# Performance work log

Hardware: AMD Instinct MI355X
Metric: run time of the kernel (lower is better)

## Reference

```python
import jax, jax.numpy as jnp
import numpy as np

B, T, D, M, H = 2048, 64, 4, 4, 256
N_STEPS = 32

# Dopri5 Butcher tableau (5th-order solution weights; f is autonomous so c is unused)
A21 = 1.0 / 5.0
A31, A32 = 3.0 / 40.0, 9.0 / 40.0
A41, A42, A43 = 44.0 / 45.0, -56.0 / 15.0, 32.0 / 9.0
A51, A52, A53, A54 = 19372.0 / 6561.0, -25360.0 / 2187.0, 64448.0 / 6561.0, -212.0 / 729.0
A61, A62, A63, A64, A65 = 9017.0 / 3168.0, -355.0 / 33.0, 46732.0 / 5247.0, 49.0 / 176.0, -5103.0 / 18656.0
B1, B3, B4, B5, B6 = 35.0 / 384.0, 500.0 / 1113.0, 125.0 / 192.0, -2187.0 / 6784.0, 11.0 / 84.0


def _gru(xin, W_ih, W_hh, b_ih, b_hh):
    # PyTorch GRU cell, gate order (r, z, n), h0 = 0
    h0 = jnp.zeros((xin.shape[0], W_hh.shape[1]), xin.dtype)

    def step(h, xt):
        gx = xt @ W_ih.T + b_ih
        gh = h @ W_hh.T + b_hh
        xr, xz, xn = jnp.split(gx, 3, axis=-1)
        hr, hz, hn = jnp.split(gh, 3, axis=-1)
        r = jax.nn.sigmoid(xr + hr)
        z = jax.nn.sigmoid(xz + hz)
        n = jnp.tanh(xn + r * hn)
        return (1.0 - z) * n + z * h, None

    h, _ = jax.lax.scan(step, h0, jnp.swapaxes(xin, 0, 1))
    return h


def _ode_f(y, p):
    W1, b1, W2, b2, W3, b3, W4, b4 = p
    h = jax.nn.selu(y @ W1.T + b1)
    h = jax.nn.selu(h @ W2.T + b2)
    h = jax.nn.selu(h @ W3.T + b3)
    return h @ W4.T + b4


def _dopri5(y0, dt, p):
    # fixed-grid Dopri5; dt is per-sample (B,1)
    def step(y, _):
        k1 = _ode_f(y, p)
        k2 = _ode_f(y + dt * (A21 * k1), p)
        k3 = _ode_f(y + dt * (A31 * k1 + A32 * k2), p)
        k4 = _ode_f(y + dt * (A41 * k1 + A42 * k2 + A43 * k3), p)
        k5 = _ode_f(y + dt * (A51 * k1 + A52 * k2 + A53 * k3 + A54 * k4), p)
        k6 = _ode_f(y + dt * (A61 * k1 + A62 * k2 + A63 * k3 + A64 * k4 + A65 * k5), p)
        y_new = y + dt * (B1 * k1 + B3 * k3 + B4 * k4 + B5 * k5 + B6 * k6)
        return y_new, None

    y, _ = jax.lax.scan(step, y0, None, length=N_STEPS)
    return y


def setup_inputs() -> dict:
    key = jax.random.key(0)
    ks = jax.random.split(key, 16)
    inp = {
        'x': jax.random.normal(ks[0], (B, T, D), jnp.float32),
        'meta': jax.random.normal(ks[1], (B, M), jnp.float32),
        'W_ih': jax.random.normal(ks[2], (3 * H, D + M), jnp.float32) * 0.05,
        'W_hh': jax.random.normal(ks[3], (3 * H, H), jnp.float32) * 0.05,
        'b_ih': jnp.zeros((3 * H,), jnp.float32),
        'b_hh': jnp.zeros((3 * H,), jnp.float32),
        'enc_W1': jax.random.normal(ks[4], (H, H), jnp.float32) * 0.05,
        'enc_b1': jnp.zeros((H,), jnp.float32),
        'enc_W2': jax.random.normal(ks[5], (2 * H, H), jnp.float32) * 0.05,
        'enc_b2': jnp.zeros((2 * H,), jnp.float32),
        'ode_W1': jax.random.normal(ks[6], (H, H), jnp.float32) * 0.001,
        'ode_b1': jnp.full((H,), 0.5, jnp.float32),
        'ode_W2': jax.random.normal(ks[7], (H, H), jnp.float32) * 0.001,
        'ode_b2': jnp.full((H,), 0.5, jnp.float32),
        'ode_W3': jax.random.normal(ks[8], (H, H), jnp.float32) * 0.001,
        'ode_b3': jnp.full((H,), 0.5, jnp.float32),
        'ode_W4': jax.random.normal(ks[9], (H, H), jnp.float32) * 0.001,
        'ode_b4': jnp.full((H,), 0.5, jnp.float32),
        'out_W': jax.random.normal(ks[10], (1, H + M), jnp.float32) * 0.05,
        'out_b': jnp.zeros((1,), jnp.float32),
    }
    return inp


def reference(x, meta, W_ih, W_hh, b_ih, b_hh, enc_W1, enc_b1, enc_W2, enc_b2,
              ode_W1, ode_b1, ode_W2, ode_b2, ode_W3, ode_b3, ode_W4, ode_b4,
              out_W, out_b):
    Bsz, Ts = x.shape[0], x.shape[1]
    Hd = enc_W1.shape[0]
    meta_t = jnp.broadcast_to(meta[:, None, :], (Bsz, Ts, meta.shape[1]))
    xin = jnp.concatenate([x, meta_t], axis=-1)  # (B, T, D+M)
    h = _gru(xin, W_ih, W_hh, b_ih, b_hh)        # (B, H)
    h = jax.nn.relu(h @ enc_W1.T + enc_b1)
    out = h @ enc_W2.T + enc_b2                  # (B, 2H)
    mean, std = out[:, :Hd], out[:, Hd:]
    eps = jax.random.normal(jax.random.key(42), mean.shape, mean.dtype)
    y0 = eps * std + mean
    times = x[:, :, 0]
    dt = (times[:, -1:] - times[:, :1]) / N_STEPS  # (B, 1) per-sample step
    p = (ode_W1, ode_b1, ode_W2, ode_b2, ode_W3, ode_b3, ode_W4, ode_b4)
    yT = _dopri5(y0, dt, p)                      # (B, H) == sol.ys[:, -1, :]
    latent = jnp.concatenate([yT, meta], axis=-1)
    return latent @ out_W.T + out_b              # (B, 1)
```

## Files before the change

### kernel.cpp

```cpp
#include <hip/hip_runtime.h>
#include <math.h>

#define HD   256
#define RB   16
#define TB   1024
#define TT   64
#define NST  32
#define BSZ  2048

typedef __attribute__((ext_vector_type(8))) short short8;
typedef __attribute__((ext_vector_type(4))) float f32x4;
typedef unsigned short ushort_t;

__device__ __forceinline__ float sigmoidf_(float x) {
    return 1.0f / (1.0f + __expf(-x));
}
__device__ __forceinline__ float tanhf_(float x) {
    float e = __expf(2.0f * x);
    return 1.0f - 2.0f / (e + 1.0f);
}
__device__ __forceinline__ float seluf_(float x) {
    const float a = 1.6732632423543772f, s = 1.0507009873554805f;
    return x > 0.0f ? s * x : s * a * (__expf(x) - 1.0f);
}
__device__ __forceinline__ float erfinvf_(float x) {
    float w = -log1pf(-x * x);
    float p;
    if (w < 5.0f) {
        w -= 2.5f;
        p = 2.81022636e-08f;
        p = fmaf(p, w, 3.43273939e-07f);
        p = fmaf(p, w, -3.5233877e-06f);
        p = fmaf(p, w, -4.39150654e-06f);
        p = fmaf(p, w, 0.00021858087f);
        p = fmaf(p, w, -0.00125372503f);
        p = fmaf(p, w, -0.00417768164f);
        p = fmaf(p, w, 0.246640727f);
        p = fmaf(p, w, 1.50140941f);
    } else {
        w = sqrtf(w) - 3.0f;
        p = -0.000200214257f;
        p = fmaf(p, w, 0.000100950558f);
        p = fmaf(p, w, 0.00134934322f);
        p = fmaf(p, w, -0.00367342844f);
        p = fmaf(p, w, 0.00573950773f);
        p = fmaf(p, w, -0.0076224613f);
        p = fmaf(p, w, 0.00943887047f);
        p = fmaf(p, w, 1.00167406f);
        p = fmaf(p, w, 2.83297682f);
    }
    return p * x;
}

#define TF_ROUND(x0, x1, R) { x0 += x1; x1 = (x1 << (R)) | (x1 >> (32 - (R))); x1 ^= x0; }

__device__ __forceinline__ void threefry_(unsigned c0, unsigned c1, unsigned& r0, unsigned& r1) {
    const unsigned ks0 = 0u, ks1 = 42u, ks2 = 0x1BD11BDAu ^ 0u ^ 42u;
    unsigned x0 = c0 + ks0, x1 = c1 + ks1;
    TF_ROUND(x0,x1,13) TF_ROUND(x0,x1,15) TF_ROUND(x0,x1,26) TF_ROUND(x0,x1,6)
    x0 += ks1; x1 += ks2 + 1u;
    TF_ROUND(x0,x1,17) TF_ROUND(x0,x1,29) TF_ROUND(x0,x1,16) TF_ROUND(x0,x1,24)
    x0 += ks2; x1 += ks0 + 2u;
    TF_ROUND(x0,x1,13) TF_ROUND(x0,x1,15) TF_ROUND(x0,x1,26) TF_ROUND(x0,x1,6)
    x0 += ks0; x1 += ks1 + 3u;
    TF_ROUND(x0,x1,17) TF_ROUND(x0,x1,29) TF_ROUND(x0,x1,16) TF_ROUND(x0,x1,24)
    x0 += ks1; x1 += ks2 + 4u;
    TF_ROUND(x0,x1,13) TF_ROUND(x0,x1,15) TF_ROUND(x0,x1,26) TF_ROUND(x0,x1,6)
    x0 += ks2; x1 += ks0 + 5u;
    r0 = x0; r1 = x1;
}

__device__ __forceinline__ float jax_normal_(unsigned i) {
    unsigned o0, o1;
    threefry_(0u, i, o0, o1);
    unsigned bits = o0 ^ o1;
    unsigned fb = (bits >> 9) | 0x3F800000u;
    float f = __uint_as_float(fb) - 1.0f;
    const float lo = -0.99999994f;
    float u = f * 2.0f + lo;
    u = fmaxf(lo, u);
    return 1.41421356237f * erfinvf_(u);
}

__device__ __forceinline__ ushort_t f2bf(float f) {
    unsigned u = __float_as_uint(f);
    return (ushort_t)((u + 0x7FFFu + ((u >> 16) & 1u)) >> 16);
}
__device__ __forceinline__ float bf2f(ushort_t u) {
    return __uint_as_float(((unsigned)u) << 16);
}

__device__ __forceinline__ int midx(int row, int k) {
    int chunk = k >> 3;
    return row * 256 + (((chunk ^ (row & 7)) << 3) | (k & 7));
}

__device__ __forceinline__ short8 ldw_f32(const float* __restrict__ Wf, int row, int k0) {
    const float4 w0 = *(const float4*)(Wf + (size_t)row * 256 + k0);
    const float4 w1 = *(const float4*)(Wf + (size_t)row * 256 + k0 + 4);
    union { ushort_t u[8]; short8 v; } bb;
    bb.u[0] = f2bf(w0.x); bb.u[1] = f2bf(w0.y); bb.u[2] = f2bf(w0.z); bb.u[3] = f2bf(w0.w);
    bb.u[4] = f2bf(w1.x); bb.u[5] = f2bf(w1.y); bb.u[6] = f2bf(w1.z); bb.u[7] = f2bf(w1.w);
    return bb.v;
}

template<int WBF>
__device__ __forceinline__ f32x4 mfma_layer(const ushort_t* __restrict__ inbf,
                                            const ushort_t* __restrict__ Wp,
                                            const float* __restrict__ Wf,
                                            const int lm, const int kb,
                                            const int wv, const int l, const int jo)
{
    f32x4 acc = {0.f, 0.f, 0.f, 0.f};
    const ushort_t* wpl = Wp + (((size_t)wv * 8) * 64 + l) * 8;
#pragma unroll
    for (int kt = 0; kt < 8; ++kt) {
        const int k0 = kt * 32 + kb * 8;
        short8 a = *(const short8*)(inbf + midx(lm, k0));
        short8 b;
        if (WBF) b = *(const short8*)(wpl + kt * 512);
        else     b = ldw_f32(Wf, jo, k0);
        acc = __builtin_amdgcn_mfma_f32_16x16x32_bf16(a, b, acc, 0, 0, 0);
    }
    return acc;
}

__global__ void cvt_k(const float* __restrict__ o1, const float* __restrict__ o2,
                      const float* __restrict__ o3, const float* __restrict__ o4,
                      const float* __restrict__ whh, const float* __restrict__ e1,
                      const float* __restrict__ e2, ushort_t* __restrict__ out) {
    int i = blockIdx.x * blockDim.x + threadIdx.x;
    if (i >= 655360) return;
    int m = i >> 16, r = i & 65535;
    const float* src;
    switch (m) {
    case 0: src = o1; break;
    case 1: src = o2; break;
    case 2: src = o3; break;
    case 3: src = o4; break;
    case 4: src = whh; break;
    case 5: src = whh + 65536; break;
    case 6: src = whh + 131072; break;
    case 7: src = e1; break;
    case 8: src = e2; break;
    default: src = e2 + 65536; break;
    }
    int e  = r & 7;
    int l  = (r >> 3) & 63;
    int kt = (r >> 9) & 7;
    int nt = r >> 12;
    int srow = nt * 16 + (l & 15);
    int sk   = kt * 32 + (l >> 4) * 8 + e;
    out[i] = f2bf(src[srow * 256 + sk]);
}

template<int WBF>
__global__ __launch_bounds__(TB, 4) void fused_kernel(
    const float* __restrict__ x,
    const float* __restrict__ meta,
    const float* __restrict__ W_ih,
    const float* __restrict__ W_hh,
    const float* __restrict__ b_ih,
    const float* __restrict__ b_hh,
    const float* __restrict__ eW1,
    const float* __restrict__ eb1,
    const float* __restrict__ eW2,
    const float* __restrict__ eb2,
    const float* __restrict__ oW1, const float* __restrict__ ob1,
    const float* __restrict__ oW2, const float* __restrict__ ob2,
    const float* __restrict__ oW3, const float* __restrict__ ob3,
    const float* __restrict__ oW4, const float* __restrict__ ob4,
    const float* __restrict__ outW,
    const float* __restrict__ outb,
    const ushort_t* __restrict__ wsbf,
    float* __restrict__ out)
{
    const int tid = threadIdx.x;
    const int t8  = tid & 255;
    const int l   = tid & 63;
    const int wv  = tid >> 6;
    const int lm  = l & 15;
    const int kb  = l >> 4;
    const int jo  = wv * 16 + lm;
    const int er4 = l >> 4;
    const int b0  = blockIdx.x * RB;

    __shared__ float h0[RB][HD];
    __shared__ float xall[RB][TT * 4];
    __shared__ float red[TB];
    __shared__ __align__(16) ushort_t mir[4][RB][256];
    __shared__ ushort_t kstb[6][RB * 256];
    __shared__ float meta_s[RB][4];
    __shared__ float dt_s[RB];

    ushort_t* YBF = &mir[0][0][0];
    ushort_t* YTB = &mir[1][0][0];
    ushort_t* T1B = &mir[2][0][0];
    ushort_t* T2B = &mir[3][0][0];
    const ushort_t* wsO1  = wsbf;
    const ushort_t* wsO2  = wsbf + 65536;
    const ushort_t* wsO3  = wsbf + 131072;
    const ushort_t* wsO4  = wsbf + 196608;
    const ushort_t* wsWr  = wsbf + 262144;
    const ushort_t* wsWz  = wsbf + 327680;
    const ushort_t* wsWn  = wsbf + 393216;
    const ushort_t* wsE1  = wsbf + 458752;
    const ushort_t* wsE2m = wsbf + 524288;
    const ushort_t* wsE2s = wsbf + 589824;

#pragma unroll
    for (int i = 0; i < 4; ++i) {
        int idx = tid + i * TB;
        int r = idx >> 8, c = idx & 255;
        xall[r][c] = x[(size_t)(b0 + r) * 256 + c];
        h0[r][c] = 0.0f;
    }
    if (tid < RB * 4) { int r = tid >> 2, mm = tid & 3; meta_s[r][mm] = meta[(b0 + r) * 4 + mm]; }
    {
        unsigned* mz = (unsigned*)&mir[0][0][0];
#pragma unroll
        for (int i = 0; i < 8; ++i) mz[tid + i * TB] = 0u;
    }
    __syncthreads();
    if (tid < RB) dt_s[tid] = (xall[tid][TT * 4 - 4] - xall[tid][0]) * (1.0f / (float)NST);

    float wxr[4], wxz[4], wxn[4];
#pragma unroll
    for (int d = 0; d < 4; ++d) {
        wxr[d] = W_ih[(size_t)jo * 8 + d];
        wxz[d] = W_ih[(size_t)(jo + 256) * 8 + d];
        wxn[d] = W_ih[(size_t)(jo + 512) * 8 + d];
    }
    float base_r[4], base_z[4], base_xn[4];
    {
        float mwr[4], mwz[4], mwn[4];
#pragma unroll
        for (int mm = 0; mm < 4; ++mm) {
            mwr[mm] = W_ih[(size_t)jo * 8 + 4 + mm];
            mwz[mm] = W_ih[(size_t)(jo + 256) * 8 + 4 + mm];
            mwn[mm] = W_ih[(size_t)(jo + 512) * 8 + 4 + mm];
        }
        const float bir = b_ih[jo], biz = b_ih[jo + 256], bin_ = b_ih[jo + 512];
        const float bhr = b_hh[jo], bhz = b_hh[jo + 256];
#pragma unroll
        for (int r = 0; r < 4; ++r) {
            const int R = er4 * 4 + r;
            float sr = bir + bhr, sz = biz + bhz, sn = bin_;
#pragma unroll
            for (int mm = 0; mm < 4; ++mm) {
                float mv = meta_s[R][mm];
                sr = fmaf(mv, mwr[mm], sr);
                sz = fmaf(mv, mwz[mm], sz);
                sn = fmaf(mv, mwn[mm], sn);
            }
            base_r[r] = sr; base_z[r] = sz; base_xn[r] = sn;
        }
    }
    const float bhn = b_hh[512 + jo];

    const ushort_t* wrl = wsWr + (((size_t)wv * 8) * 64 + l) * 8;
    const ushort_t* wzl = wsWz + (((size_t)wv * 8) * 64 + l) * 8;
    const ushort_t* wnl = wsWn + (((size_t)wv * 8) * 64 + l) * 8;
    int p = 0;
#pragma unroll 1
    for (int t = 0; t < TT; ++t) {
        const ushort_t* YHp = &mir[p][0][0];
        f32x4 aR = {0.f,0.f,0.f,0.f}, aZ = {0.f,0.f,0.f,0.f}, aN = {0.f,0.f,0.f,0.f};
#pragma unroll 2
        for (int kt = 0; kt < 8; ++kt) {
            const int k0 = kt * 32 + kb * 8;
            short8 a = *(const short8*)(YHp + midx(lm, k0));
            short8 b;
            if (WBF) b = *(const short8*)(wrl + kt * 512);
            else     b = ldw_f32(W_hh, jo, k0);
            aR = __builtin_amdgcn_mfma_f32_16x16x32_bf16(a, b, aR, 0, 0, 0);
            if (WBF) b = *(const short8*)(wzl + kt * 512);
            else     b = ldw_f32(W_hh, jo + 256, k0);
            aZ = __builtin_amdgcn_mfma_f32_16x16x32_bf16(a, b, aZ, 0, 0, 0);
            if (WBF) b = *(const short8*)(wnl + kt * 512);
            else     b = ldw_f32(W_hh, jo + 512, k0);
            aN = __builtin_amdgcn_mfma_f32_16x16x32_bf16(a, b, aN, 0, 0, 0);
        }
        {
            ushort_t* YHn = &mir[p ^ 1][0][0];
#pragma unroll
            for (int r = 0; r < 4; ++r) {
                const int R = er4 * 4 + r;
                float xr = base_r[r], xz = base_z[r], xn = base_xn[r];
#pragma unroll
                for (int d = 0; d < 4; ++d) {
                    float xv = xall[R][t * 4 + d];
                    xr = fmaf(xv, wxr[d], xr);
                    xz = fmaf(xv, wxz[d], xz);
                    xn = fmaf(xv, wxn[d], xn);
                }
                float rg = sigmoidf_(xr + aR[r]);
                float zg = sigmoidf_(xz + aZ[r]);
                float ng = tanhf_(fmaf(rg, aN[r] + bhn, xn));
                float hp = h0[R][jo];
                float hnew = fmaf(zg, hp - ng, ng);
                h0[R][jo] = hnew;
                YHn[midx(R, jo)] = f2bf(hnew);
            }
        }
        __syncthreads();
        p ^= 1;
    }

    {
        f32x4 acc = mfma_layer<WBF>(YBF, wsE1, eW1, lm, kb, wv, l, jo);
        {
            const float eb1j = eb1[jo];
#pragma unroll
            for (int r = 0; r < 4; ++r)
                T1B[midx(er4 * 4 + r, jo)] = f2bf(fmaxf(acc[r] + eb1j, 0.0f));
        }
        __syncthreads();

        f32x4 aM = mfma_layer<WBF>(T1B, wsE2m, eW2, lm, kb, wv, l, jo);
        f32x4 aS = mfma_layer<WBF>(T1B, wsE2s, eW2 + 65536, lm, kb, wv, l, jo);
        {
            const float bm = eb2[jo], bs = eb2[256 + jo];
#pragma unroll
            for (int r = 0; r < 4; ++r) {
                const int row = er4 * 4 + r;
                float e = jax_normal_((unsigned)((b0 + row) * HD + jo));
                float y0v = fmaf(e, aS[r] + bs, aM[r] + bm);
                h0[row][jo] = y0v;
                YBF[midx(row, jo)] = f2bf(y0v);
            }
        }
        __syncthreads();
    }

    const float A21 = (float)(1.0/5.0);
    const float A31 = (float)(3.0/40.0),      A32 = (float)(9.0/40.0);
    const float A41 = (float)(44.0/45.0),     A42 = (float)(-56.0/15.0),    A43 = (float)(32.0/9.0);
    const float A51 = (float)(19372.0/6561.0),A52 = (float)(-25360.0/2187.0),
                A53 = (float)(64448.0/6561.0),A54 = (float)(-212.0/729.0);
    const float A61 = (float)(9017.0/3168.0), A62 = (float)(-355.0/33.0),
                A63 = (float)(46732.0/5247.0),A64 = (float)(49.0/176.0),    A65 = (float)(-5103.0/18656.0);
    const float B1f = (float)(35.0/384.0),    B3f = (float)(500.0/1113.0),  B4f = (float)(125.0/192.0),
                B5f = (float)(-2187.0/6784.0),B6f = (float)(11.0/84.0);

    const float o1b = ob1[jo], o2b = ob2[jo], o3b = ob3[jo], o4b = ob4[jo];
    float dtv[4];
#pragma unroll
    for (int r = 0; r < 4; ++r) dtv[r] = dt_s[er4 * 4 + r];

#pragma unroll 1
    for (int st = 0; st < NST; ++st) {
#pragma unroll 1
        for (int stage = 0; stage < 6; ++stage) {
            const ushort_t* in0 = (stage == 0) ? YBF : YTB;
            f32x4 acc = mfma_layer<WBF>(in0, wsO1, oW1, lm, kb, wv, l, jo);
            {
#pragma unroll
                for (int r = 0; r < 4; ++r)
                    T1B[midx(er4 * 4 + r, jo)] = f2bf(seluf_(acc[r] + o1b));
            }
            __syncthreads();
            acc = mfma_layer<WBF>(T1B, wsO2, oW2, lm, kb, wv, l, jo);
            {
#pragma unroll
                for (int r = 0; r < 4; ++r)
                    T2B[midx(er4 * 4 + r, jo)] = f2bf(seluf_(acc[r] + o2b));
            }
            __syncthreads();
            acc = mfma_layer<WBF>(T2B, wsO3, oW3, lm, kb, wv, l, jo);
            {
#pragma unroll
                for (int r = 0; r < 4; ++r)
                    T1B[midx(er4 * 4 + r, jo)] = f2bf(seluf_(acc[r] + o3b));
            }
            __syncthreads();
            acc = mfma_layer<WBF>(T1B, wsO4, oW4, lm, kb, wv, l, jo);
            {
#pragma unroll
                for (int r = 0; r < 4; ++r) {
                    const int row = er4 * 4 + r;
                    const int ki = row * 256 + jo;
                    const float kc = acc[r] + o4b;
                    kstb[stage][ki] = f2bf(kc);
                    const float yv = h0[row][jo];
                    float sm;
                    switch (stage) {
                    case 0:
                        sm = A21 * kc;
                        break;
                    case 1: {
                        float k1v = bf2f(kstb[0][ki]);
                        sm = fmaf(A32, kc, A31 * k1v);
                        break; }
                    case 2: {
                        float k1v = bf2f(kstb[0][ki]), k2v = bf2f(kstb[1][ki]);
                        sm = fmaf(A43, kc, fmaf(A42, k2v, A41 * k1v));
                        break; }
                    case 3: {
                        float k1v = bf2f(kstb[0][ki]), k2v = bf2f(kstb[1][ki]);
                        float k3v = bf2f(kstb[2][ki]);
                        sm = fmaf(A54, kc, fmaf(A53, k3v, fmaf(A52, k2v, A51 * k1v)));
                        break; }
                    case 4: {
                        float k1v = bf2f(kstb[0][ki]), k2v = bf2f(kstb[1][ki]);
                        float k3v = bf2f(kstb[2][ki]), k4v = bf2f(kstb[3][ki]);
                        sm = fmaf(A65, kc, fmaf(A64, k4v,
                             fmaf(A63, k3v, fmaf(A62, k2v, A61 * k1v))));
                        break; }
                    default: {
                        float k1v = bf2f(kstb[0][ki]), k3v = bf2f(kstb[2][ki]);
                        float k4v = bf2f(kstb[3][ki]), k5v = bf2f(kstb[4][ki]);
                        sm = fmaf(B6f, kc, fmaf(B5f, k5v,
                             fmaf(B4f, k4v, fmaf(B3f, k3v, B1f * k1v))));
                        break; }
                    }
                    const float yn = fmaf(dtv[r], sm, yv);
                    if (stage < 5) {
                        YTB[midx(row, jo)] = f2bf(yn);
                    } else {
                        h0[row][jo] = yn;
                        YBF[midx(row, jo)] = f2bf(yn);
                    }
                }
            }
            __syncthreads();
        }
    }

#pragma unroll 1
    for (int rp4 = 0; rp4 < 4; ++rp4) {
        const int R = rp4 * 4 + (tid >> 8);
        red[tid] = h0[R][t8] * outW[t8];
        __syncthreads();
        for (int sw = 128; sw > 0; sw >>= 1) {
            if (t8 < sw) red[tid] += red[tid + sw];
            __syncthreads();
        }
        if (t8 == 0) {
            float acc = red[tid] + outb[0];
#pragma unroll
            for (int mm = 0; mm < 4; ++mm) acc = fmaf(meta_s[R][mm], outW[HD + mm], acc);
            out[b0 + R] = acc;
        }
        __syncthreads();
    }
}

extern "C" void kernel_launch(void* const* d_in, const int* in_sizes, int n_in,
                              void* d_out, int out_size, void* d_ws, size_t ws_size,
                              hipStream_t stream) {
    const float* x    = (const float*)d_in[0];
    const float* meta = (const float*)d_in[1];
    const float* W_ih = (const float*)d_in[2];
    const float* W_hh = (const float*)d_in[3];
    const float* b_ih = (const float*)d_in[4];
    const float* b_hh = (const float*)d_in[5];
    const float* eW1  = (const float*)d_in[6];
    const float* eb1  = (const float*)d_in[7];
    const float* eW2  = (const float*)d_in[8];
    const float* eb2  = (const float*)d_in[9];
    const float* oW1  = (const float*)d_in[10];
    const float* ob1  = (const float*)d_in[11];
    const float* oW2  = (const float*)d_in[12];
    const float* ob2  = (const float*)d_in[13];
    const float* oW3  = (const float*)d_in[14];
    const float* ob3  = (const float*)d_in[15];
    const float* oW4  = (const float*)d_in[16];
    const float* ob4  = (const float*)d_in[17];
    const float* outW = (const float*)d_in[18];
    const float* outb = (const float*)d_in[19];

    const size_t need = (size_t)655360 * sizeof(ushort_t);
    const bool wbf = (d_ws != nullptr) && (ws_size >= need);

    if (wbf) {
        cvt_k<<<2560, 256, 0, stream>>>(oW1, oW2, oW3, oW4, W_hh, eW1, eW2,
                                        (ushort_t*)d_ws);
        fused_kernel<1><<<BSZ / RB, TB, 0, stream>>>(x, meta, W_ih, W_hh, b_ih, b_hh,
                                                     eW1, eb1, eW2, eb2,
                                                     oW1, ob1, oW2, ob2, oW3, ob3, oW4, ob4,
                                                     outW, outb, (const ushort_t*)d_ws,
                                                     (float*)d_out);
    } else {
        fused_kernel<0><<<BSZ / RB, TB, 0, stream>>>(x, meta, W_ih, W_hh, b_ih, b_hh,
                                                     eW1, eb1, eW2, eb2,
                                                     oW1, ob1, oW2, ob2, oW3, ob3, oW4, ob4,
                                                     outW, outb, (const ushort_t*)nullptr,
                                                     (float*)d_out);
    }
}
```

Before: 1.739 ms.

## Process 32 rows per block and keep GRU/ODE state in registers

Doubles the rows per block from 16 to 32, so each loaded weight fragment feeds two MFMAs, one per 16-row half. The GRU hidden state, the ODE state y and the six Dopri5 stage vectors now live in per-thread registers instead of shared-memory arrays, which removes the h0 and kstb buffers and their LDS round trips. The intent is to amortise weight loads and cut shared-memory traffic per barrier. In exchange the grid halves to 64 blocks on an already underfilled device, and register pressure rises, which risks spills or lower occupancy.

```diff
diff --git a/kernel.cpp b/kernel.cpp
--- a/kernel.cpp
+++ b/kernel.cpp
@@ -2,7 +2,7 @@
 #include <math.h>
 
 #define HD   256
-#define RB   16
+#define RB   32
 #define TB   1024
 #define TT   64
 #define NST  32
@@ -86,9 +86,6 @@
     unsigned u = __float_as_uint(f);
     return (ushort_t)((u + 0x7FFFu + ((u >> 16) & 1u)) >> 16);
 }
-__device__ __forceinline__ float bf2f(ushort_t u) {
-    return __uint_as_float(((unsigned)u) << 16);
-}
 
 __device__ __forceinline__ int midx(int row, int k) {
     int chunk = k >> 3;
@@ -105,24 +102,27 @@
 }
 
 template<int WBF>
-__device__ __forceinline__ f32x4 mfma_layer(const ushort_t* __restrict__ inbf,
+__device__ __forceinline__ void mfma_layer2(const ushort_t* __restrict__ inbf,
                                             const ushort_t* __restrict__ Wp,
                                             const float* __restrict__ Wf,
                                             const int lm, const int kb,
-                                            const int wv, const int l, const int jo)
+                                            const int wv, const int l, const int jo,
+                                            f32x4& r0, f32x4& r1)
 {
-    f32x4 acc = {0.f, 0.f, 0.f, 0.f};
+    f32x4 a0 = {0.f, 0.f, 0.f, 0.f}, a1 = {0.f, 0.f, 0.f, 0.f};
     const ushort_t* wpl = Wp + (((size_t)wv * 8) * 64 + l) * 8;
 #pragma unroll
     for (int kt = 0; kt < 8; ++kt) {
         const int k0 = kt * 32 + kb * 8;
-        short8 a = *(const short8*)(inbf + midx(lm, k0));
+        short8 A0 = *(const short8*)(inbf + midx(lm, k0));
+        short8 A1 = *(const short8*)(inbf + midx(16 + lm, k0));
         short8 b;
         if (WBF) b = *(const short8*)(wpl + kt * 512);
         else     b = ldw_f32(Wf, jo, k0);
-        acc = __builtin_amdgcn_mfma_f32_16x16x32_bf16(a, b, acc, 0, 0, 0);
-    }
-    return acc;
+        a0 = __builtin_amdgcn_mfma_f32_16x16x32_bf16(A0, b, a0, 0, 0, 0);
+        a1 = __builtin_amdgcn_mfma_f32_16x16x32_bf16(A1, b, a1, 0, 0, 0);
+    }
+    r0 = a0; r1 = a1;
 }
 
 __global__ void cvt_k(const float* __restrict__ o1, const float* __restrict__ o2,
@@ -185,11 +185,9 @@
     const int er4 = l >> 4;
     const int b0  = blockIdx.x * RB;
 
-    __shared__ float h0[RB][HD];
-    __shared__ float xall[RB][TT * 4];
+    __shared__ float xall[RB][HD];
     __shared__ float red[TB];
     __shared__ __align__(16) ushort_t mir[4][RB][256];
-    __shared__ ushort_t kstb[6][RB * 256];
     __shared__ float meta_s[RB][4];
     __shared__ float dt_s[RB];
 
@@ -209,20 +207,19 @@
     const ushort_t* wsE2s = wsbf + 589824;
 
 #pragma unroll
-    for (int i = 0; i < 4; ++i) {
+    for (int i = 0; i < 8; ++i) {
         int idx = tid + i * TB;
         int r = idx >> 8, c = idx & 255;
         xall[r][c] = x[(size_t)(b0 + r) * 256 + c];
-        h0[r][c] = 0.0f;
     }
     if (tid < RB * 4) { int r = tid >> 2, mm = tid & 3; meta_s[r][mm] = meta[(b0 + r) * 4 + mm]; }
     {
         unsigned* mz = (unsigned*)&mir[0][0][0];
 #pragma unroll
-        for (int i = 0; i < 8; ++i) mz[tid + i * TB] = 0u;
+        for (int i = 0; i < 4; ++i) mz[tid + i * TB] = 0u;
     }
     __syncthreads();
-    if (tid < RB) dt_s[tid] = (xall[tid][TT * 4 - 4] - xall[tid][0]) * (1.0f / (float)NST);
+    if (tid < RB) dt_s[tid] = (xall[tid][HD - 4] - xall[tid][0]) * (1.0f / (float)NST);
 
     float wxr[4], wxz[4], wxn[4];
 #pragma unroll
@@ -231,7 +228,7 @@
         wxz[d] = W_ih[(size_t)(jo + 256) * 8 + d];
         wxn[d] = W_ih[(size_t)(jo + 512) * 8 + d];
     }
-    float base_r[4], base_z[4], base_xn[4];
+    float base_r[8], base_z[8], base_xn[8];
     {
         float mwr[4], mwz[4], mwn[4];
 #pragma unroll
@@ -243,8 +240,8 @@
         const float bir = b_ih[jo], biz = b_ih[jo + 256], bin_ = b_ih[jo + 512];
         const float bhr = b_hh[jo], bhz = b_hh[jo + 256];
 #pragma unroll
-        for (int r = 0; r < 4; ++r) {
-            const int R = er4 * 4 + r;
+        for (int rr = 0; rr < 8; ++rr) {
+            const int R = (rr < 4) ? (er4 * 4 + rr) : (16 + er4 * 4 + rr - 4);
             float sr = bir + bhr, sz = biz + bhz, sn = bin_;
 #pragma unroll
             for (int mm = 0; mm < 4; ++mm) {
@@ -253,10 +250,14 @@
                 sz = fmaf(mv, mwz[mm], sz);
                 sn = fmaf(mv, mwn[mm], sn);
             }
-            base_r[r] = sr; base_z[r] = sz; base_xn[r] = sn;
+            base_r[rr] = sr; base_z[rr] = sz; base_xn[rr] = sn;
         }
     }
     const float bhn = b_hh[512 + jo];
+
+    float hreg[8];
+#pragma unroll
+    for (int rr = 0; rr < 8; ++rr) hreg[rr] = 0.0f;
 
     const ushort_t* wrl = wsWr + (((size_t)wv * 8) * 64 + l) * 8;
     const ushort_t* wzl = wsWz + (((size_t)wv * 8) * 64 + l) * 8;
@@ -265,70 +266,81 @@
 #pragma unroll 1
     for (int t = 0; t < TT; ++t) {
         const ushort_t* YHp = &mir[p][0][0];
-        f32x4 aR = {0.f,0.f,0.f,0.f}, aZ = {0.f,0.f,0.f,0.f}, aN = {0.f,0.f,0.f,0.f};
+        f32x4 aR0 = {0,0,0,0}, aR1 = {0,0,0,0};
+        f32x4 aZ0 = {0,0,0,0}, aZ1 = {0,0,0,0};
+        f32x4 aN0 = {0,0,0,0}, aN1 = {0,0,0,0};
 #pragma unroll 2
         for (int kt = 0; kt < 8; ++kt) {
             const int k0 = kt * 32 + kb * 8;
-            short8 a = *(const short8*)(YHp + midx(lm, k0));
+            short8 A0 = *(const short8*)(YHp + midx(lm, k0));
+            short8 A1 = *(const short8*)(YHp + midx(16 + lm, k0));
             short8 b;
             if (WBF) b = *(const short8*)(wrl + kt * 512);
             else     b = ldw_f32(W_hh, jo, k0);
-            aR = __builtin_amdgcn_mfma_f32_16x16x32_bf16(a, b, aR, 0, 0, 0);
+            aR0 = __builtin_amdgcn_mfma_f32_16x16x32_bf16(A0, b, aR0, 0, 0, 0);
+            aR1 = __builtin_amdgcn_mfma_f32_16x16x32_bf16(A1, b, aR1, 0, 0, 0);
             if (WBF) b = *(const short8*)(wzl + kt * 512);
             else     b = ldw_f32(W_hh, jo + 256, k0);
-            aZ = __builtin_amdgcn_mfma_f32_16x16x32_bf16(a, b, aZ, 0, 0, 0);
+            aZ0 = __builtin_amdgcn_mfma_f32_16x16x32_bf16(A0, b, aZ0, 0, 0, 0);
+            aZ1 = __builtin_amdgcn_mfma_f32_16x16x32_bf16(A1, b, aZ1, 0, 0, 0);
             if (WBF) b = *(const short8*)(wnl + kt * 512);
             else     b = ldw_f32(W_hh, jo + 512, k0);
-            aN = __builtin_amdgcn_mfma_f32_16x16x32_bf16(a, b, aN, 0, 0, 0);
-        }
-        {
-            ushort_t* YHn = &mir[p ^ 1][0][0];
-#pragma unroll
-            for (int r = 0; r < 4; ++r) {
-                const int R = er4 * 4 + r;
-                float xr = base_r[r], xz = base_z[r], xn = base_xn[r];
-#pragma unroll
-                for (int d = 0; d < 4; ++d) {
-                    float xv = xall[R][t * 4 + d];
-                    xr = fmaf(xv, wxr[d], xr);
-                    xz = fmaf(xv, wxz[d], xz);
-                    xn = fmaf(xv, wxn[d], xn);
-                }
-                float rg = sigmoidf_(xr + aR[r]);
-                float zg = sigmoidf_(xz + aZ[r]);
-                float ng = tanhf_(fmaf(rg, aN[r] + bhn, xn));
-                float hp = h0[R][jo];
-                float hnew = fmaf(zg, hp - ng, ng);
-                h0[R][jo] = hnew;
-                YHn[midx(R, jo)] = f2bf(hnew);
+            aN0 = __builtin_amdgcn_mfma_f32_16x16x32_bf16(A0, b, aN0, 0, 0, 0);
+            aN1 = __builtin_amdgcn_mfma_f32_16x16x32_bf16(A1, b, aN1, 0, 0, 0);
+        }
+        ushort_t* YHn = &mir[p ^ 1][0][0];
+#pragma unroll
+        for (int rr = 0; rr < 8; ++rr) {
+            const int R = (rr < 4) ? (er4 * 4 + rr) : (16 + er4 * 4 + rr - 4);
+            const float aRv = (rr < 4) ? aR0[rr] : aR1[rr - 4];
+            const float aZv = (rr < 4) ? aZ0[rr] : aZ1[rr - 4];
+            const float aNv = (rr < 4) ? aN0[rr] : aN1[rr - 4];
+            float xr = base_r[rr], xz = base_z[rr], xn = base_xn[rr];
+#pragma unroll
+            for (int d = 0; d < 4; ++d) {
+                float xv = xall[R][t * 4 + d];
+                xr = fmaf(xv, wxr[d], xr);
+                xz = fmaf(xv, wxz[d], xz);
+                xn = fmaf(xv, wxn[d], xn);
             }
+            float rg = sigmoidf_(xr + aRv);
+            float zg = sigmoidf_(xz + aZv);
+            float ng = tanhf_(fmaf(rg, aNv + bhn, xn));
+            float hnew = fmaf(zg, hreg[rr] - ng, ng);
+            hreg[rr] = hnew;
+            YHn[midx(R, jo)] = f2bf(hnew);
         }
         __syncthreads();
         p ^= 1;
     }
 
+    float yreg[8];
+
     {
-        f32x4 acc = mfma_layer<WBF>(YBF, wsE1, eW1, lm, kb, wv, l, jo);
-        {
-            const float eb1j = eb1[jo];
-#pragma unroll
-            for (int r = 0; r < 4; ++r)
-                T1B[midx(er4 * 4 + r, jo)] = f2bf(fmaxf(acc[r] + eb1j, 0.0f));
+        f32x4 c0, c1;
+        mfma_layer2<WBF>(YBF, wsE1, eW1, lm, kb, wv, l, jo, c0, c1);
+        const float eb1j = eb1[jo];
+#pragma unroll
+        for (int rr = 0; rr < 8; ++rr) {
+            const int R = (rr < 4) ? (er4 * 4 + rr) : (16 + er4 * 4 + rr - 4);
+            const float v = (rr < 4) ? c0[rr] : c1[rr - 4];
+            T1B[midx(R, jo)] = f2bf(fmaxf(v + eb1j, 0.0f));
         }
         __syncthreads();
 
-        f32x4 aM = mfma_layer<WBF>(T1B, wsE2m, eW2, lm, kb, wv, l, jo);
-        f32x4 aS = mfma_layer<WBF>(T1B, wsE2s, eW2 + 65536, lm, kb, wv, l, jo);
-        {
-            const float bm = eb2[jo], bs = eb2[256 + jo];
-#pragma unroll
-            for (int r = 0; r < 4; ++r) {
-                const int row = er4 * 4 + r;
-                float e = jax_normal_((unsigned)((b0 + row) * HD + jo));
-                float y0v = fmaf(e, aS[r] + bs, aM[r] + bm);
-                h0[row][jo] = y0v;
-                YBF[midx(row, jo)] = f2bf(y0v);
-            }
+        f32x4 m0, m1, s0, s1;
+        mfma_layer2<WBF>(T1B, wsE2m, eW2, lm, kb, wv, l, jo, m0, m1);
+        mfma_layer2<WBF>(T1B, wsE2s, eW2 + 65536, lm, kb, wv, l, jo, s0, s1);
+        const float bm = eb2[jo], bs = eb2[256 + jo];
+#pragma unroll
+        for (int rr = 0; rr < 8; ++rr) {
+            const int R = (rr < 4) ? (er4 * 4 + rr) : (16 + er4 * 4 + rr - 4);
+            const float mv = ((rr < 4) ? m0[rr] : m1[rr - 4]) + bm;
+            const float sv = ((rr < 4) ? s0[rr] : s1[rr - 4]) + bs;
+            float e = jax_normal_((unsigned)((b0 + R) * HD + jo));
+            float y0v = fmaf(e, sv, mv);
+            yreg[rr] = y0v;
+            YBF[midx(R, jo)] = f2bf(y0v);
         }
         __syncthreads();
     }
@@ -344,93 +356,100 @@
                 B5f = (float)(-2187.0/6784.0),B6f = (float)(11.0/84.0);
 
     const float o1b = ob1[jo], o2b = ob2[jo], o3b = ob3[jo], o4b = ob4[jo];
-    float dtv[4];
-#pragma unroll
-    for (int r = 0; r < 4; ++r) dtv[r] = dt_s[er4 * 4 + r];
+    float dtv[8];
+#pragma unroll
+    for (int rr = 0; rr < 8; ++rr) {
+        const int R = (rr < 4) ? (er4 * 4 + rr) : (16 + er4 * 4 + rr - 4);
+        dtv[rr] = dt_s[R];
+    }
+    float k1[8], k2[8], k3[8], k4[8], k5[8], k6[8];
 
 #pragma unroll 1
     for (int st = 0; st < NST; ++st) {
 #pragma unroll 1
         for (int stage = 0; stage < 6; ++stage) {
             const ushort_t* in0 = (stage == 0) ? YBF : YTB;
-            f32x4 acc = mfma_layer<WBF>(in0, wsO1, oW1, lm, kb, wv, l, jo);
-            {
-#pragma unroll
-                for (int r = 0; r < 4; ++r)
-                    T1B[midx(er4 * 4 + r, jo)] = f2bf(seluf_(acc[r] + o1b));
+            f32x4 c0, c1;
+            mfma_layer2<WBF>(in0, wsO1, oW1, lm, kb, wv, l, jo, c0, c1);
+#pragma unroll
+            for (int rr = 0; rr < 8; ++rr) {
+                const int R = (rr < 4) ? (er4 * 4 + rr) : (16 + er4 * 4 + rr - 4);
+                const float v = (rr < 4) ? c0[rr] : c1[rr - 4];
+                T1B[midx(R, jo)] = f2bf(seluf_(v + o1b));
             }
             __syncthreads();
-            acc = mfma_layer<WBF>(T1B, wsO2, oW2, lm, kb, wv, l, jo);
-            {
-#pragma unroll
-                for (int r = 0; r < 4; ++r)
-                    T2B[midx(er4 * 4 + r, jo)] = f2bf(seluf_(acc[r] + o2b));
+            mfma_layer2<WBF>(T1B, wsO2, oW2, lm, kb, wv, l, jo, c0, c1);
+#pragma unroll
+            for (int rr = 0; rr < 8; ++rr) {
+                const int R = (rr < 4) ? (er4 * 4 + rr) : (16 + er4 * 4 + rr - 4);
+                const float v = (rr < 4) ? c0[rr] : c1[rr - 4];
+                T2B[midx(R, jo)] = f2bf(seluf_(v + o2b));
             }
             __syncthreads();
-            acc = mfma_layer<WBF>(T2B, wsO3, oW3, lm, kb, wv, l, jo);
-            {
-#pragma unroll
-                for (int r = 0; r < 4; ++r)
-                    T1B[midx(er4 * 4 + r, jo)] = f2bf(seluf_(acc[r] + o3b));
+            mfma_layer2<WBF>(T2B, wsO3, oW3, lm, kb, wv, l, jo, c0, c1);
+#pragma unroll
+            for (int rr = 0; rr < 8; ++rr) {
+                const int R = (rr < 4) ? (er4 * 4 + rr) : (16 + er4 * 4 + rr - 4);
+                const float v = (rr < 4) ? c0[rr] : c1[rr - 4];
+                T1B[midx(R, jo)] = f2bf(seluf_(v + o3b));
             }
             __syncthreads();
-            acc = mfma_layer<WBF>(T1B, wsO4, oW4, lm, kb, wv, l, jo);
-            {
-#pragma unroll
-                for (int r = 0; r < 4; ++r) {
-                    const int row = er4 * 4 + r;
-                    const int ki = row * 256 + jo;
-                    const float kc = acc[r] + o4b;
-                    kstb[stage][ki] = f2bf(kc);
-                    const float yv = h0[row][jo];
-                    float sm;
-                    switch (stage) {
-                    case 0:
-                        sm = A21 * kc;
-                        break;
-                    case 1: {
-                        float k1v = bf2f(kstb[0][ki]);
-                        sm = fmaf(A32, kc, A31 * k1v);
-                        break; }
-                    case 2: {
-                        float k1v = bf2f(kstb[0][ki]), k2v = bf2f(kstb[1][ki]);
-                        sm = fmaf(A43, kc, fmaf(A42, k2v, A41 * k1v));
-                        break; }
-                    case 3: {
-                        float k1v = bf2f(kstb[0][ki]), k2v = bf2f(kstb[1][ki]);
-                        float k3v = bf2f(kstb[2][ki]);
-                        sm = fmaf(A54, kc, fmaf(A53, k3v, fmaf(A52, k2v, A51 * k1v)));
-                        break; }
-                    case 4: {
-                        float k1v = bf2f(kstb[0][ki]), k2v = bf2f(kstb[1][ki]);
-                        float k3v = bf2f(kstb[2][ki]), k4v = bf2f(kstb[3][ki]);
-                        sm = fmaf(A65, kc, fmaf(A64, k4v,
-                             fmaf(A63, k3v, fmaf(A62, k2v, A61 * k1v))));
-                        break; }
-                    default: {
-                        float k1v = bf2f(kstb[0][ki]), k3v = bf2f(kstb[2][ki]);
-                        float k4v = bf2f(kstb[3][ki]), k5v = bf2f(kstb[4][ki]);
-                        sm = fmaf(B6f, kc, fmaf(B5f, k5v,
-                             fmaf(B4f, k4v, fmaf(B3f, k3v, B1f * k1v))));
-                        break; }
-                    }
-                    const float yn = fmaf(dtv[r], sm, yv);
-                    if (stage < 5) {
-                        YTB[midx(row, jo)] = f2bf(yn);
-                    } else {
-                        h0[row][jo] = yn;
-                        YBF[midx(row, jo)] = f2bf(yn);
-                    }
+            mfma_layer2<WBF>(T1B, wsO4, oW4, lm, kb, wv, l, jo, c0, c1);
+#pragma unroll
+            for (int rr = 0; rr < 8; ++rr) {
+                const int R = (rr < 4) ? (er4 * 4 + rr) : (16 + er4 * 4 + rr - 4);
+                const float kc = ((rr < 4) ? c0[rr] : c1[rr - 4]) + o4b;
+                float sm;
+                switch (stage) {
+                case 0:
+                    k1[rr] = kc;
+                    sm = A21 * kc;
+                    break;
+                case 1:
+                    k2[rr] = kc;
+                    sm = fmaf(A32, kc, A31 * k1[rr]);
+                    break;
+                case 2:
+                    k3[rr] = kc;
+                    sm = fmaf(A43, kc, fmaf(A42, k2[rr], A41 * k1[rr]));
+                    break;
+                case 3:
+                    k4[rr] = kc;
+                    sm = fmaf(A54, kc, fmaf(A53, k3[rr], fmaf(A52, k2[rr], A51 * k1[rr])));
+                    break;
+                case 4:
+                    k5[rr] = kc;
+                    sm = fmaf(A65, kc, fmaf(A64, k4[rr],
+                         fmaf(A63, k3[rr], fmaf(A62, k2[rr], A61 * k1[rr]))));
+                    break;
+                default:
+                    k6[rr] = kc;
+                    sm = fmaf(B6f, kc, fmaf(B5f, k5[rr],
+                         fmaf(B4f, k4[rr], fmaf(B3f, k3[rr], B1f * k1[rr]))));
+                    break;
+                }
+                const float yn = fmaf(dtv[rr], sm, (stage < 5) ? yreg[rr] : yreg[rr]);
+                if (stage < 5) {
+                    YTB[midx(R, jo)] = f2bf(yn);
+                } else {
+                    yreg[rr] = yn;
+                    YBF[midx(R, jo)] = f2bf(yn);
                 }
             }
             __syncthreads();
         }
     }
 
+#pragma unroll
+    for (int rr = 0; rr < 8; ++rr) {
+        const int R = (rr < 4) ? (er4 * 4 + rr) : (16 + er4 * 4 + rr - 4);
+        xall[R][jo] = yreg[rr];
+    }
+    __syncthreads();
 #pragma unroll 1
-    for (int rp4 = 0; rp4 < 4; ++rp4) {
+    for (int rp4 = 0; rp4 < 8; ++rp4) {
         const int R = rp4 * 4 + (tid >> 8);
-        red[tid] = h0[R][t8] * outW[t8];
+        red[tid] = xall[R][t8] * outW[t8];
         __syncthreads();
         for (int sw = 128; sw > 0; sw >>= 1) {
             if (t8 < sw) red[tid] += red[tid + sw];
```

New measurement: 3.067 ms. 1.76x slower.
